# Performance work log

Measured on AMD Instinct MI355X. Metric: run time of the kernel, lower is better.

## Reference

```python
import jax, jax.numpy as jnp
import numpy as np

N_NODES = 100000
N_EDGES = 1600000
D_IN = 128
D_OUT = 128


def setup_inputs() -> dict:
    key = jax.random.key(0)
    k1, k2, k3, k4, k5, k6 = jax.random.split(key, 6)
    x = jax.random.normal(k1, (N_NODES, D_IN), dtype=jnp.float32)
    rows = jax.random.randint(k2, (N_EDGES,), 0, N_NODES, dtype=jnp.int32)
    cols = jax.random.randint(k3, (N_EDGES,), 0, N_NODES, dtype=jnp.int32)
    vals = jax.random.uniform(k4, (N_EDGES,), dtype=jnp.float32)
    # nn.Linear init: U(-1/sqrt(in), 1/sqrt(in))
    bound = 1.0 / np.sqrt(D_IN)
    W = jax.random.uniform(k5, (D_IN, D_OUT), minval=-bound, maxval=bound, dtype=jnp.float32)
    b = jax.random.uniform(k6, (D_OUT,), minval=-bound, maxval=bound, dtype=jnp.float32)
    return {"x": x, "rows": rows, "cols": cols, "vals": vals, "W": W, "b": b}


def reference(x, rows, cols, vals, W, b):
    # support = fc1(x)  -> [N, D_OUT]
    support = x @ W + b
    # output = adj @ support, adj in COO form (rows, cols, vals)
    msg = support[cols] * vals[:, None]          # [E, D_OUT] gather + scale
    out = jax.ops.segment_sum(msg, rows, num_segments=N_NODES)  # scatter-add
    return out
```

## Files before the change

kernel.cpp:

```cpp
#include <hip/hip_runtime.h>

#define D 128
#define NB_MAX 1024
#define CHN 6250
#define CAP 2560
#define SP 136

typedef short short8 __attribute__((ext_vector_type(8)));
typedef float floatx4 __attribute__((ext_vector_type(4)));

__device__ inline unsigned short f2bf(float f) {
  unsigned u = __float_as_uint(f);
  u += 0x7fffu + ((u >> 16) & 1u);
  return (unsigned short)(u >> 16);
}

__global__ __launch_bounds__(1024) void prep_kernel(
    const float* __restrict__ W, unsigned short* __restrict__ wf,
    const float* __restrict__ x, unsigned short* __restrict__ xh,
    const int* __restrict__ rows, int* __restrict__ chunk_hist,
    int n_edges, int nchunks, int nb, int total_elems) {
  __shared__ int h[NB_MAX];
  const int bid = blockIdx.x;
  const int t = threadIdx.x;

  if (bid < nchunks) {
    h[t] = 0;
    __syncthreads();
    int lo = bid * CHN;
    int hi = min(lo + CHN, n_edges);
    for (int i = lo + t; i < hi; i += 1024) atomicAdd(&h[rows[i] >> 7], 1);
    __syncthreads();
    if (t < nb) chunk_hist[bid * nb + t] = h[t];
    return;
  }

  if (bid < nchunks + 2) {
    int tid = (bid - nchunks) * 1024 + t;
    int ks = tid >> 9;
    int rem = tid & 511;
    int nt = rem >> 6;
    int lane = rem & 63;
    int n = nt * 16 + (lane & 15);
    int k0 = ks * 32 + (lane >> 4) * 8;
    unsigned short v[8];
#pragma unroll
    for (int j = 0; j < 8; ++j) v[j] = f2bf(W[(k0 + j) * D + n]);
    uint4 o;
    o.x = (unsigned)v[0] | ((unsigned)v[1] << 16);
    o.y = (unsigned)v[2] | ((unsigned)v[3] << 16);
    o.z = (unsigned)v[4] | ((unsigned)v[5] << 16);
    o.w = (unsigned)v[6] | ((unsigned)v[7] << 16);
    ((uint4*)wf)[tid] = o;
    return;
  }

  int idx = (bid - nchunks - 2) * 1024 + t;
  if (idx * 16 < total_elems) {
    const float4* x4 = (const float4*)x;
    uint4* xh4 = (uint4*)xh;
#pragma unroll
    for (int j = 0; j < 2; ++j) {
      float4 a = x4[idx * 4 + 2 * j];
      float4 c = x4[idx * 4 + 2 * j + 1];
      uint4 o;
      o.x = (unsigned)f2bf(a.x) | ((unsigned)f2bf(a.y) << 16);
      o.y = (unsigned)f2bf(a.z) | ((unsigned)f2bf(a.w) << 16);
      o.z = (unsigned)f2bf(c.x) | ((unsigned)f2bf(c.y) << 16);
      o.w = (unsigned)f2bf(c.z) | ((unsigned)f2bf(c.w) << 16);
      xh4[idx * 2 + j] = o;
    }
  }
}

__global__ __launch_bounds__(1024) void partition_kernel(
    const int* __restrict__ rows, const int* __restrict__ cols,
    const float* __restrict__ vals, const int* __restrict__ chunk_hist,
    int* __restrict__ bucket_off, int2* __restrict__ tmp,
    int n_edges, int nchunks, int nb) {
  __shared__ int pscn[NB_MAX];
  __shared__ int h[NB_MAX];
  __shared__ int base_s[NB_MAX];
  const int c = blockIdx.x;
  const int t = threadIdx.x;

  int tot = 0, pre = 0;
  if (t < nb) {
    for (int cc = 0; cc < nchunks; ++cc) {
      int v = chunk_hist[cc * nb + t];
      tot += v;
      pre += (cc < c) ? v : 0;
    }
  }
  pscn[t] = (t < nb) ? tot : 0;
  __syncthreads();
  for (int d = 1; d < 1024; d <<= 1) {
    int v = (t >= d) ? pscn[t - d] : 0;
    __syncthreads();
    pscn[t] += v;
    __syncthreads();
  }
  int excl = (t == 0) ? 0 : pscn[t - 1];
  if (c == 0) {
    if (t < nb) bucket_off[t] = excl;
    if (t == 0) bucket_off[nb] = pscn[nb - 1];
  }
  base_s[t] = excl + pre;
  h[t] = 0;
  __syncthreads();

  int lo = c * CHN;
  int hi = min(lo + CHN, n_edges);
  for (int i = lo + t; i < hi; i += 1024) {
    int r = rows[i];
    int bkt = r >> 7;
    int l = atomicAdd(&h[bkt], 1);
    tmp[base_s[bkt] + l] =
        make_int2(((r & 127) << 17) | cols[i], __float_as_int(vals[i]));
  }
}

__global__ __launch_bounds__(1024, 8) void gather_gemm_kernel(
    const uint2* __restrict__ xh, const unsigned short* __restrict__ wf,
    const float* __restrict__ bias, const int* __restrict__ bucket_off,
    const int2* __restrict__ tmp, float* __restrict__ out, int n_nodes) {
  __shared__ __align__(16) char U[67584];
  __shared__ int cnt[128];
  __shared__ int scn[128];
  __shared__ int rs[129];
  __shared__ float rowsum[128];
  unsigned short* ys = (unsigned short*)U;
  int2* ebuf = (int2*)U;
  int2* sbuf = (int2*)(U + 34816);
  unsigned short* wfs = (unsigned short*)(U + 34816);
  const int t = threadIdx.x;
  const int b = blockIdx.x;

  const uint4* wf4 = (const uint4*)wf;
  uint4 wfr0 = wf4[t];
  uint4 wfr1 = wf4[t + 1024];

  const int lo = bucket_off[b];
  const int ne = bucket_off[b + 1] - lo;
  const int slot = t >> 5;
  const int lane = t & 31;

  if (ne <= CAP) {
    if (t < 128) cnt[t] = 0;
    __syncthreads();
    for (int i = t; i < ne; i += 1024) {
      int2 p = tmp[lo + i];
      ebuf[i] = p;
      atomicAdd(&cnt[((unsigned)p.x) >> 17], 1);
    }
    __syncthreads();
    if (t < 128) scn[t] = cnt[t];
    __syncthreads();
#pragma unroll
    for (int d = 1; d < 128; d <<= 1) {
      int v = (t < 128 && t >= d) ? scn[t - d] : 0;
      __syncthreads();
      if (t < 128) scn[t] += v;
      __syncthreads();
    }
    if (t < 128) {
      rs[t] = (t == 0) ? 0 : scn[t - 1];
      cnt[t] = 0;
    }
    __syncthreads();
    if (t == 0) rs[128] = scn[127];
    for (int i = t; i < ne; i += 1024) {
      int2 p = ebuf[i];
      int r = ((unsigned)p.x) >> 17;
      int l = atomicAdd(&cnt[r], 1);
      sbuf[rs[r] + l] = p;
    }
    __syncthreads();
#pragma unroll
    for (int rr = 0; rr < 4; ++rr) {
      int row = slot + (rr << 5);
      int s = rs[row], e = rs[row + 1];
      float4 acc = make_float4(0.f, 0.f, 0.f, 0.f);
      float rsum = 0.f;
      int i = s;
      for (; i + 4 <= e; i += 4) {
        int2 p0 = sbuf[i + 0];
        int2 p1 = sbuf[i + 1];
        int2 p2 = sbuf[i + 2];
        int2 p3 = sbuf[i + 3];
        uint2 s0 = xh[((size_t)(p0.x & 0x1FFFF) << 5) + lane];
        uint2 s1 = xh[((size_t)(p1.x & 0x1FFFF) << 5) + lane];
        uint2 s2 = xh[((size_t)(p2.x & 0x1FFFF) << 5) + lane];
        uint2 s3 = xh[((size_t)(p3.x & 0x1FFFF) << 5) + lane];
        float v0 = __int_as_float(p0.y), v1 = __int_as_float(p1.y);
        float v2 = __int_as_float(p2.y), v3 = __int_as_float(p3.y);
        rsum += v0 + v1 + v2 + v3;
        acc.x += v0 * __uint_as_float(s0.x << 16);
        acc.y += v0 * __uint_as_float(s0.x & 0xffff0000u);
        acc.z += v0 * __uint_as_float(s0.y << 16);
        acc.w += v0 * __uint_as_float(s0.y & 0xffff0000u);
        acc.x += v1 * __uint_as_float(s1.x << 16);
        acc.y += v1 * __uint_as_float(s1.x & 0xffff0000u);
        acc.z += v1 * __uint_as_float(s1.y << 16);
        acc.w += v1 * __uint_as_float(s1.y & 0xffff0000u);
        acc.x += v2 * __uint_as_float(s2.x << 16);
        acc.y += v2 * __uint_as_float(s2.x & 0xffff0000u);
        acc.z += v2 * __uint_as_float(s2.y << 16);
        acc.w += v2 * __uint_as_float(s2.y & 0xffff0000u);
        acc.x += v3 * __uint_as_float(s3.x << 16);
        acc.y += v3 * __uint_as_float(s3.x & 0xffff0000u);
        acc.z += v3 * __uint_as_float(s3.y << 16);
        acc.w += v3 * __uint_as_float(s3.y & 0xffff0000u);
      }
      for (; i < e; ++i) {
        int2 p = sbuf[i];
        float v = __int_as_float(p.y);
        uint2 sv = xh[((size_t)(p.x & 0x1FFFF) << 5) + lane];
        rsum += v;
        acc.x += v * __uint_as_float(sv.x << 16);
        acc.y += v * __uint_as_float(sv.x & 0xffff0000u);
        acc.z += v * __uint_as_float(sv.y << 16);
        acc.w += v * __uint_as_float(sv.y & 0xffff0000u);
      }
      unsigned u0 = (unsigned)f2bf(acc.x) | ((unsigned)f2bf(acc.y) << 16);
      unsigned u1 = (unsigned)f2bf(acc.z) | ((unsigned)f2bf(acc.w) << 16);
      *((uint2*)(ys + row * SP + lane * 4)) = make_uint2(u0, u1);
      if (lane == 0) rowsum[row] = rsum;
    }
  } else {
#pragma unroll
    for (int rr = 0; rr < 4; ++rr) {
      int row = slot + (rr << 5);
      float4 acc = make_float4(0.f, 0.f, 0.f, 0.f);
      float rsum = 0.f;
      for (int i = 0; i < ne; ++i) {
        int2 p = tmp[lo + i];
        if ((int)(((unsigned)p.x) >> 17) != row) continue;
        float v = __int_as_float(p.y);
        uint2 sv = xh[((size_t)(p.x & 0x1FFFF) << 5) + lane];
        rsum += v;
        acc.x += v * __uint_as_float(sv.x << 16);
        acc.y += v * __uint_as_float(sv.x & 0xffff0000u);
        acc.z += v * __uint_as_float(sv.y << 16);
        acc.w += v * __uint_as_float(sv.y & 0xffff0000u);
      }
      unsigned u0 = (unsigned)f2bf(acc.x) | ((unsigned)f2bf(acc.y) << 16);
      unsigned u1 = (unsigned)f2bf(acc.z) | ((unsigned)f2bf(acc.w) << 16);
      *((uint2*)(ys + row * SP + lane * 4)) = make_uint2(u0, u1);
      if (lane == 0) rowsum[row] = rsum;
    }
  }
  __syncthreads();

  uint4* wfs4 = (uint4*)wfs;
  wfs4[t] = wfr0;
  wfs4[t + 1024] = wfr1;
  __syncthreads();

  const int l64 = t & 63;
  const int w = t >> 6;
  const int m = l64 & 15, q = l64 >> 4;
  const int rb = (w & 3) * 32;
  const int cb = (w >> 2) * 32;

  floatx4 acc2[2][2];
#pragma unroll
  for (int rt = 0; rt < 2; ++rt)
#pragma unroll
    for (int ct = 0; ct < 2; ++ct) {
      acc2[rt][ct][0] = 0.f; acc2[rt][ct][1] = 0.f;
      acc2[rt][ct][2] = 0.f; acc2[rt][ct][3] = 0.f;
    }

#pragma unroll
  for (int ks = 0; ks < 4; ++ks) {
    short8 af[2], bfr[2];
#pragma unroll
    for (int rt = 0; rt < 2; ++rt)
      af[rt] = *((const short8*)(ys + (rb + rt * 16 + m) * SP + ks * 32 + q * 8));
#pragma unroll
    for (int ct = 0; ct < 2; ++ct) {
      int nt = (cb >> 4) + ct;
      bfr[ct] = *((const short8*)(wfs + ((ks * 8 + nt) * 64 + l64) * 8));
    }
#pragma unroll
    for (int rt = 0; rt < 2; ++rt)
#pragma unroll
      for (int ct = 0; ct < 2; ++ct)
        acc2[rt][ct] = __builtin_amdgcn_mfma_f32_16x16x32_bf16(
            af[rt], bfr[ct], acc2[rt][ct], 0, 0, 0);
  }

  float b0 = bias[cb + m];
  float b1 = bias[cb + 16 + m];
#pragma unroll
  for (int rt = 0; rt < 2; ++rt)
#pragma unroll
    for (int ct = 0; ct < 2; ++ct) {
      float bc = ct ? b1 : b0;
#pragma unroll
      for (int r = 0; r < 4; ++r) {
        int row = rb + rt * 16 + q * 4 + r;
        int col = cb + ct * 16 + m;
        int node = (b << 7) + row;
        if (node < n_nodes)
          out[(size_t)node * D + col] = acc2[rt][ct][r] + rowsum[row] * bc;
      }
    }
}

extern "C" void kernel_launch(void* const* d_in, const int* in_sizes, int n_in,
                              void* d_out, int out_size, void* d_ws, size_t ws_size,
                              hipStream_t stream) {
  const float* x    = (const float*)d_in[0];
  const int*   rows = (const int*)d_in[1];
  const int*   cols = (const int*)d_in[2];
  const float* vals = (const float*)d_in[3];
  const float* W    = (const float*)d_in[4];
  const float* b    = (const float*)d_in[5];
  float* out = (float*)d_out;

  int n_nodes = in_sizes[0] / D;
  int n_edges = in_sizes[1];
  int nb = (n_nodes + 127) >> 7;
  int nchunks = (n_edges + CHN - 1) / CHN;
  int total_elems = n_nodes * D;

  char* ws = (char*)d_ws;
  unsigned short* xh = (unsigned short*)(ws);
  int2* tmp          = (int2*)(ws + 25600000);
  char* mb           = ws + 38400000;
  int* bucket_off    = (int*)(mb);
  unsigned short* wf = (unsigned short*)(mb + 4096);
  int* chunk_hist    = (int*)out;

  int ncast = (total_elems + 16383) / 16384;
  prep_kernel<<<dim3(nchunks + 2 + ncast), dim3(1024), 0, stream>>>(
      W, wf, x, xh, rows, chunk_hist, n_edges, nchunks, nb, total_elems);

  partition_kernel<<<dim3(nchunks), dim3(1024), 0, stream>>>(
      rows, cols, vals, chunk_hist, bucket_off, tmp, n_edges, nchunks, nb);

  gather_gemm_kernel<<<dim3(nb), dim3(1024), 0, stream>>>(
      (const uint2*)xh, wf, b, bucket_off, tmp, out, n_nodes);
}
```

Baseline: 283.0 us.

## Replace single-pass bucket partition with two-level radix partition and separate x cast

The edge partition by destination bucket now runs in two passes. The first scatters edges into 49 superbuckets of 2048 rows, then a second kernel splits each superbucket into its 16 row buckets, keeping per-chunk order. The goal is to cut the scattered writes across ~782 buckets that made the old single pass poorly coalesced. The bf16 cast of x moves to its own kernel that reuses the tmp1 workspace after partitioning, and the gather inner loop is unrolled from 4 to 8 edges for more memory-level parallelism. The cost is an extra kernel launch plus an extra read and write pass over the edge list.

```diff
diff --git a/kernel.cpp b/kernel.cpp
--- a/kernel.cpp
+++ b/kernel.cpp
@@ -2,7 +2,8 @@
 
 #define D 128
 #define NB_MAX 1024
-#define CHN 6250
+#define NSB_STRIDE 64
+#define CHN 4096
 #define CAP 2560
 #define SP 136
 
@@ -15,28 +16,16 @@
   return (unsigned short)(u >> 16);
 }
 
-__global__ __launch_bounds__(1024) void prep_kernel(
+__global__ __launch_bounds__(256) void prep_kernel(
     const float* __restrict__ W, unsigned short* __restrict__ wf,
-    const float* __restrict__ x, unsigned short* __restrict__ xh,
     const int* __restrict__ rows, int* __restrict__ chunk_hist,
-    int n_edges, int nchunks, int nb, int total_elems) {
+    int* __restrict__ chunk_sb, int n_edges, int nb, int nsb) {
   __shared__ int h[NB_MAX];
   const int bid = blockIdx.x;
   const int t = threadIdx.x;
 
-  if (bid < nchunks) {
-    h[t] = 0;
-    __syncthreads();
-    int lo = bid * CHN;
-    int hi = min(lo + CHN, n_edges);
-    for (int i = lo + t; i < hi; i += 1024) atomicAdd(&h[rows[i] >> 7], 1);
-    __syncthreads();
-    if (t < nb) chunk_hist[bid * nb + t] = h[t];
-    return;
-  }
-
-  if (bid < nchunks + 2) {
-    int tid = (bid - nchunks) * 1024 + t;
+  if (bid < 8) {
+    int tid = bid * 256 + t;
     int ks = tid >> 9;
     int rem = tid & 511;
     int nt = rem >> 6;
@@ -55,68 +44,149 @@
     return;
   }
 
-  int idx = (bid - nchunks - 2) * 1024 + t;
-  if (idx * 16 < total_elems) {
-    const float4* x4 = (const float4*)x;
-    uint4* xh4 = (uint4*)xh;
-#pragma unroll
-    for (int j = 0; j < 2; ++j) {
-      float4 a = x4[idx * 4 + 2 * j];
-      float4 c = x4[idx * 4 + 2 * j + 1];
-      uint4 o;
-      o.x = (unsigned)f2bf(a.x) | ((unsigned)f2bf(a.y) << 16);
-      o.y = (unsigned)f2bf(a.z) | ((unsigned)f2bf(a.w) << 16);
-      o.z = (unsigned)f2bf(c.x) | ((unsigned)f2bf(c.y) << 16);
-      o.w = (unsigned)f2bf(c.z) | ((unsigned)f2bf(c.w) << 16);
-      xh4[idx * 2 + j] = o;
-    }
-  }
-}
-
-__global__ __launch_bounds__(1024) void partition_kernel(
+  int c = bid - 8;
+  for (int i = t; i < NB_MAX; i += 256) h[i] = 0;
+  __syncthreads();
+  int lo = c * CHN;
+  int hi = min(lo + CHN, n_edges);
+  for (int i = lo + t; i < hi; i += 256) atomicAdd(&h[rows[i] >> 7], 1);
+  __syncthreads();
+  for (int b = t; b < nb; b += 256) chunk_hist[c * nb + b] = h[b];
+  if (t < nsb) {
+    int s = 0;
+#pragma unroll
+    for (int k = 0; k < 16; ++k) s += h[t * 16 + k];
+    chunk_sb[c * NSB_STRIDE + t] = s;
+  }
+}
+
+__global__ __launch_bounds__(1024) void p1_kernel(
     const int* __restrict__ rows, const int* __restrict__ cols,
     const float* __restrict__ vals, const int* __restrict__ chunk_hist,
-    int* __restrict__ bucket_off, int2* __restrict__ tmp,
-    int n_edges, int nchunks, int nb) {
-  __shared__ int pscn[NB_MAX];
-  __shared__ int h[NB_MAX];
-  __shared__ int base_s[NB_MAX];
+    const int* __restrict__ chunk_sb, int* __restrict__ bucket_off,
+    int2* __restrict__ tmp1, int n_edges, int nchunks, int nb, int nsb) {
   const int c = blockIdx.x;
   const int t = threadIdx.x;
 
-  int tot = 0, pre = 0;
-  if (t < nb) {
+  if (c == nchunks) {
+    __shared__ int pscn[1024];
+    int tot = 0;
+    if (t < nb)
+      for (int cc = 0; cc < nchunks; ++cc) tot += chunk_hist[cc * nb + t];
+    pscn[t] = (t < nb) ? tot : 0;
+    __syncthreads();
+    for (int d = 1; d < 1024; d <<= 1) {
+      int v = (t >= d) ? pscn[t - d] : 0;
+      __syncthreads();
+      pscn[t] += v;
+      __syncthreads();
+    }
+    if (t < nb) bucket_off[t] = (t == 0) ? 0 : pscn[t - 1];
+    if (t == 0) bucket_off[nb] = pscn[nb - 1];
+    return;
+  }
+
+  __shared__ int sbt[NSB_STRIDE];
+  __shared__ int sbo[NSB_STRIDE];
+  __shared__ int base_s[NSB_STRIDE];
+  __shared__ int h[NSB_STRIDE];
+  if (t < nsb) {
+    int tot = 0, pre = 0;
     for (int cc = 0; cc < nchunks; ++cc) {
-      int v = chunk_hist[cc * nb + t];
+      int v = chunk_sb[cc * NSB_STRIDE + t];
       tot += v;
       pre += (cc < c) ? v : 0;
     }
-  }
-  pscn[t] = (t < nb) ? tot : 0;
-  __syncthreads();
-  for (int d = 1; d < 1024; d <<= 1) {
-    int v = (t >= d) ? pscn[t - d] : 0;
-    __syncthreads();
-    pscn[t] += v;
-    __syncthreads();
-  }
-  int excl = (t == 0) ? 0 : pscn[t - 1];
-  if (c == 0) {
-    if (t < nb) bucket_off[t] = excl;
-    if (t == 0) bucket_off[nb] = pscn[nb - 1];
-  }
-  base_s[t] = excl + pre;
-  h[t] = 0;
+    sbt[t] = tot;
+    base_s[t] = pre;
+    h[t] = 0;
+  }
+  __syncthreads();
+  if (t == 0) {
+    int run = 0;
+    for (int s = 0; s < nsb; ++s) { sbo[s] = run; run += sbt[s]; }
+  }
+  __syncthreads();
+  if (t < nsb) base_s[t] += sbo[t];
   __syncthreads();
 
   int lo = c * CHN;
   int hi = min(lo + CHN, n_edges);
   for (int i = lo + t; i < hi; i += 1024) {
     int r = rows[i];
-    int bkt = r >> 7;
-    int l = atomicAdd(&h[bkt], 1);
-    tmp[base_s[bkt] + l] =
-        make_int2(((r & 127) << 17) | cols[i], __float_as_int(vals[i]));
+    int s = r >> 11;
+    int l = atomicAdd(&h[s], 1);
+    tmp1[base_s[s] + l] =
+        make_int2(((r & 2047) << 17) | cols[i], __float_as_int(vals[i]));
+  }
+}
+
+__global__ __launch_bounds__(1024) void p2_kernel(
+    const int* __restrict__ chunk_hist, const int* __restrict__ chunk_sb,
+    const int* __restrict__ bucket_off, const int2* __restrict__ tmp1,
+    int2* __restrict__ tmp2, int nchunks, int nb, int nsb) {
+  __shared__ int wbase[16];
+  __shared__ int h[16];
+  __shared__ int cnt16[16];
+  __shared__ int ab[2];
+  const int s = blockIdx.x >> 4;
+  const int j = blockIdx.x & 15;
+  const int t = threadIdx.x;
+  const int c0 = (nchunks * j) >> 4;
+  const int c1 = (nchunks * (j + 1)) >> 4;
+
+  if (t < 16) {
+    int b = (s << 4) + t;
+    int pre = 0, cnt = 0;
+    if (b < nb) {
+      for (int cc = 0; cc < c1; ++cc) {
+        int v = chunk_hist[cc * nb + b];
+        pre += (cc < c0) ? v : 0;
+        cnt += (cc >= c0) ? v : 0;
+      }
+      wbase[t] = bucket_off[b] + pre;
+    } else {
+      wbase[t] = 0;
+    }
+    cnt16[t] = cnt;
+    h[t] = 0;
+  }
+  __syncthreads();
+  if (t == 0) {
+    int sbstart = bucket_off[s << 4];
+    int pre_sum = 0, cnt_sum = 0;
+    for (int k = 0; k < 16; ++k) {
+      int b = (s << 4) + k;
+      if (b < nb) pre_sum += wbase[k] - bucket_off[b];
+      cnt_sum += cnt16[k];
+    }
+    ab[0] = sbstart + pre_sum;
+    ab[1] = sbstart + pre_sum + cnt_sum;
+  }
+  __syncthreads();
+  const int a = ab[0], bend = ab[1];
+
+  for (int i = a + t; i < bend; i += 1024) {
+    int2 p = tmp1[i];
+    int bi = (((unsigned)p.x) >> 24) & 15;
+    int l = atomicAdd(&h[bi], 1);
+    tmp2[wbase[bi] + l] = make_int2(p.x & 0x00FFFFFF, p.y);
+  }
+}
+
+__global__ __launch_bounds__(1024) void xcast_kernel(
+    const float* __restrict__ x, unsigned int* __restrict__ xh2, int total4) {
+  const float4* x4 = (const float4*)x;
+  int base = blockIdx.x * 4096;
+#pragma unroll
+  for (int k = 0; k < 4; ++k) {
+    int i = base + k * 1024 + threadIdx.x;
+    if (i < total4) {
+      float4 v = x4[i];
+      unsigned lo = (unsigned)f2bf(v.x) | ((unsigned)f2bf(v.y) << 16);
+      unsigned hi = (unsigned)f2bf(v.z) | ((unsigned)f2bf(v.w) << 16);
+      ((uint2*)xh2)[i] = make_uint2(lo, hi);
+    }
   }
 }
 
@@ -183,18 +253,28 @@
       float4 acc = make_float4(0.f, 0.f, 0.f, 0.f);
       float rsum = 0.f;
       int i = s;
-      for (; i + 4 <= e; i += 4) {
+      for (; i + 8 <= e; i += 8) {
         int2 p0 = sbuf[i + 0];
         int2 p1 = sbuf[i + 1];
         int2 p2 = sbuf[i + 2];
         int2 p3 = sbuf[i + 3];
+        int2 p4 = sbuf[i + 4];
+        int2 p5 = sbuf[i + 5];
+        int2 p6 = sbuf[i + 6];
+        int2 p7 = sbuf[i + 7];
         uint2 s0 = xh[((size_t)(p0.x & 0x1FFFF) << 5) + lane];
         uint2 s1 = xh[((size_t)(p1.x & 0x1FFFF) << 5) + lane];
         uint2 s2 = xh[((size_t)(p2.x & 0x1FFFF) << 5) + lane];
         uint2 s3 = xh[((size_t)(p3.x & 0x1FFFF) << 5) + lane];
+        uint2 s4 = xh[((size_t)(p4.x & 0x1FFFF) << 5) + lane];
+        uint2 s5 = xh[((size_t)(p5.x & 0x1FFFF) << 5) + lane];
+        uint2 s6 = xh[((size_t)(p6.x & 0x1FFFF) << 5) + lane];
+        uint2 s7 = xh[((size_t)(p7.x & 0x1FFFF) << 5) + lane];
         float v0 = __int_as_float(p0.y), v1 = __int_as_float(p1.y);
         float v2 = __int_as_float(p2.y), v3 = __int_as_float(p3.y);
-        rsum += v0 + v1 + v2 + v3;
+        float v4 = __int_as_float(p4.y), v5 = __int_as_float(p5.y);
+        float v6 = __int_as_float(p6.y), v7 = __int_as_float(p7.y);
+        rsum += v0 + v1 + v2 + v3 + v4 + v5 + v6 + v7;
         acc.x += v0 * __uint_as_float(s0.x << 16);
         acc.y += v0 * __uint_as_float(s0.x & 0xffff0000u);
         acc.z += v0 * __uint_as_float(s0.y << 16);
@@ -211,6 +291,22 @@
         acc.y += v3 * __uint_as_float(s3.x & 0xffff0000u);
         acc.z += v3 * __uint_as_float(s3.y << 16);
         acc.w += v3 * __uint_as_float(s3.y & 0xffff0000u);
+        acc.x += v4 * __uint_as_float(s4.x << 16);
+        acc.y += v4 * __uint_as_float(s4.x & 0xffff0000u);
+        acc.z += v4 * __uint_as_float(s4.y << 16);
+        acc.w += v4 * __uint_as_float(s4.y & 0xffff0000u);
+        acc.x += v5 * __uint_as_float(s5.x << 16);
+        acc.y += v5 * __uint_as_float(s5.x & 0xffff0000u);
+        acc.z += v5 * __uint_as_float(s5.y << 16);
+        acc.w += v5 * __uint_as_float(s5.y & 0xffff0000u);
+        acc.x += v6 * __uint_as_float(s6.x << 16);
+        acc.y += v6 * __uint_as_float(s6.x & 0xffff0000u);
+        acc.z += v6 * __uint_as_float(s6.y << 16);
+        acc.w += v6 * __uint_as_float(s6.y & 0xffff0000u);
+        acc.x += v7 * __uint_as_float(s7.x << 16);
+        acc.y += v7 * __uint_as_float(s7.x & 0xffff0000u);
+        acc.z += v7 * __uint_as_float(s7.y << 16);
+        acc.w += v7 * __uint_as_float(s7.y & 0xffff0000u);
       }
       for (; i < e; ++i) {
         int2 p = sbuf[i];
@@ -323,24 +419,34 @@
   int n_nodes = in_sizes[0] / D;
   int n_edges = in_sizes[1];
   int nb = (n_nodes + 127) >> 7;
+  int nsb = (nb + 15) >> 4;
   int nchunks = (n_edges + CHN - 1) / CHN;
   int total_elems = n_nodes * D;
 
   char* ws = (char*)d_ws;
+  int2* tmp1         = (int2*)(ws);
   unsigned short* xh = (unsigned short*)(ws);
-  int2* tmp          = (int2*)(ws + 25600000);
+  int2* tmp2         = (int2*)(ws + 25600000);
   char* mb           = ws + 38400000;
   int* bucket_off    = (int*)(mb);
   unsigned short* wf = (unsigned short*)(mb + 4096);
   int* chunk_hist    = (int*)out;
-
-  int ncast = (total_elems + 16383) / 16384;
-  prep_kernel<<<dim3(nchunks + 2 + ncast), dim3(1024), 0, stream>>>(
-      W, wf, x, xh, rows, chunk_hist, n_edges, nchunks, nb, total_elems);
-
-  partition_kernel<<<dim3(nchunks), dim3(1024), 0, stream>>>(
-      rows, cols, vals, chunk_hist, bucket_off, tmp, n_edges, nchunks, nb);
+  int* chunk_sb      = (int*)((char*)out + 2000000);
+
+  prep_kernel<<<dim3(8 + nchunks), dim3(256), 0, stream>>>(
+      W, wf, rows, chunk_hist, chunk_sb, n_edges, nb, nsb);
+
+  p1_kernel<<<dim3(nchunks + 1), dim3(1024), 0, stream>>>(
+      rows, cols, vals, chunk_hist, chunk_sb, bucket_off, tmp1,
+      n_edges, nchunks, nb, nsb);
+
+  p2_kernel<<<dim3(nsb * 16), dim3(1024), 0, stream>>>(
+      chunk_hist, chunk_sb, bucket_off, tmp1, tmp2, nchunks, nb, nsb);
+
+  int total4 = total_elems >> 2;
+  xcast_kernel<<<dim3((total4 + 4095) / 4096), dim3(1024), 0, stream>>>(
+      x, (unsigned int*)xh, total4);
 
   gather_gemm_kernel<<<dim3(nb), dim3(1024), 0, stream>>>(
-      (const uint2*)xh, wf, b, bucket_off, tmp, out, n_nodes);
-}
+      (const uint2*)xh, wf, b, bucket_off, tmp2, out, n_nodes);
+}
```

Result: slower. 466.5 us (+64.8%).

## Partition edges into coarse 2048-row superbuckets and filter per block in gather kernel

Applied to the files above, without the earlier changes.

Replaces the fine 128-row bucket histogram and partition (782 buckets × 256 chunks) with coarse 2048-row superbuckets (49 of them), making the histogram and prefix-scan work much smaller. Each gather block now scans its whole superbucket and keeps only the edges for its 128-row sub-bucket. Blocks are mapped so that the blocks sharing a superbucket sit on the same XCD to help L2 reuse. The trade-off is that each superbucket's edge list is read 16 times, and the filter adds shared atomics. The bf16 cast of x is also reshaped into per-float4 work items.

```diff
diff --git a/kernel.cpp b/kernel.cpp
--- a/kernel.cpp
+++ b/kernel.cpp
@@ -1,8 +1,9 @@
 #include <hip/hip_runtime.h>
 
 #define D 128
-#define NB_MAX 1024
-#define CHN 6250
+#define SBMAX 64
+#define CSTRIDE 400
+#define CHN 4096
 #define CAP 2560
 #define SP 136
 
@@ -17,26 +18,15 @@
 
 __global__ __launch_bounds__(1024) void prep_kernel(
     const float* __restrict__ W, unsigned short* __restrict__ wf,
-    const float* __restrict__ x, unsigned short* __restrict__ xh,
-    const int* __restrict__ rows, int* __restrict__ chunk_hist,
-    int n_edges, int nchunks, int nb, int total_elems) {
-  __shared__ int h[NB_MAX];
+    const float* __restrict__ x, unsigned int* __restrict__ xh2,
+    const int* __restrict__ rows, int* __restrict__ chunk_sb,
+    int n_edges, int nchunks, int nsb, int total4) {
+  __shared__ int h[SBMAX];
   const int bid = blockIdx.x;
   const int t = threadIdx.x;
 
-  if (bid < nchunks) {
-    h[t] = 0;
-    __syncthreads();
-    int lo = bid * CHN;
-    int hi = min(lo + CHN, n_edges);
-    for (int i = lo + t; i < hi; i += 1024) atomicAdd(&h[rows[i] >> 7], 1);
-    __syncthreads();
-    if (t < nb) chunk_hist[bid * nb + t] = h[t];
-    return;
-  }
-
-  if (bid < nchunks + 2) {
-    int tid = (bid - nchunks) * 1024 + t;
+  if (bid < 2) {
+    int tid = bid * 1024 + t;
     int ks = tid >> 9;
     int rem = tid & 511;
     int nt = rem >> 6;
@@ -55,105 +45,144 @@
     return;
   }
 
-  int idx = (bid - nchunks - 2) * 1024 + t;
-  if (idx * 16 < total_elems) {
-    const float4* x4 = (const float4*)x;
-    uint4* xh4 = (uint4*)xh;
-#pragma unroll
-    for (int j = 0; j < 2; ++j) {
-      float4 a = x4[idx * 4 + 2 * j];
-      float4 c = x4[idx * 4 + 2 * j + 1];
-      uint4 o;
-      o.x = (unsigned)f2bf(a.x) | ((unsigned)f2bf(a.y) << 16);
-      o.y = (unsigned)f2bf(a.z) | ((unsigned)f2bf(a.w) << 16);
-      o.z = (unsigned)f2bf(c.x) | ((unsigned)f2bf(c.y) << 16);
-      o.w = (unsigned)f2bf(c.z) | ((unsigned)f2bf(c.w) << 16);
-      xh4[idx * 2 + j] = o;
-    }
-  }
-}
-
-__global__ __launch_bounds__(1024) void partition_kernel(
+  if (bid < 2 + nchunks) {
+    if (t < SBMAX) h[t] = 0;
+    __syncthreads();
+    int c = bid - 2;
+    int lo = c * CHN;
+    int hi = min(lo + CHN, n_edges);
+    for (int i = lo + t; i < hi; i += 1024) atomicAdd(&h[rows[i] >> 11], 1);
+    __syncthreads();
+    if (t < nsb) chunk_sb[t * CSTRIDE + c] = h[t];
+    return;
+  }
+
+  const float4* x4 = (const float4*)x;
+  int base = (bid - 2 - nchunks) * 4096;
+#pragma unroll
+  for (int k = 0; k < 4; ++k) {
+    int i = base + k * 1024 + t;
+    if (i < total4) {
+      float4 v = x4[i];
+      unsigned lo = (unsigned)f2bf(v.x) | ((unsigned)f2bf(v.y) << 16);
+      unsigned hi = (unsigned)f2bf(v.z) | ((unsigned)f2bf(v.w) << 16);
+      ((uint2*)xh2)[i] = make_uint2(lo, hi);
+    }
+  }
+}
+
+__global__ __launch_bounds__(1024) void p1_kernel(
     const int* __restrict__ rows, const int* __restrict__ cols,
-    const float* __restrict__ vals, const int* __restrict__ chunk_hist,
-    int* __restrict__ bucket_off, int2* __restrict__ tmp,
-    int n_edges, int nchunks, int nb) {
-  __shared__ int pscn[NB_MAX];
-  __shared__ int h[NB_MAX];
-  __shared__ int base_s[NB_MAX];
+    const float* __restrict__ vals, const int* __restrict__ chunk_sb,
+    int* __restrict__ sb_off, int2* __restrict__ tmp1,
+    int n_edges, int nchunks, int nsb) {
+  __shared__ int ptot[1024];
+  __shared__ int ppre[1024];
+  __shared__ int sbt[SBMAX];
+  __shared__ int sbo[SBMAX + 1];
+  __shared__ int base_s[SBMAX];
+  __shared__ int h[SBMAX];
   const int c = blockIdx.x;
   const int t = threadIdx.x;
 
-  int tot = 0, pre = 0;
-  if (t < nb) {
-    for (int cc = 0; cc < nchunks; ++cc) {
-      int v = chunk_hist[cc * nb + t];
-      tot += v;
-      pre += (cc < c) ? v : 0;
-    }
-  }
-  pscn[t] = (t < nb) ? tot : 0;
-  __syncthreads();
-  for (int d = 1; d < 1024; d <<= 1) {
-    int v = (t >= d) ? pscn[t - d] : 0;
-    __syncthreads();
-    pscn[t] += v;
-    __syncthreads();
-  }
-  int excl = (t == 0) ? 0 : pscn[t - 1];
-  if (c == 0) {
-    if (t < nb) bucket_off[t] = excl;
-    if (t == 0) bucket_off[nb] = pscn[nb - 1];
-  }
-  base_s[t] = excl + pre;
-  h[t] = 0;
+  {
+    int s = t >> 4, g = t & 15;
+    int tp = 0, pp = 0;
+    if (s < nsb) {
+      int strip = (nchunks + 15) >> 4;
+      int a = g * strip;
+      int b2 = min(a + strip, nchunks);
+      const int* rowp = chunk_sb + s * CSTRIDE;
+      for (int cc = a; cc < b2; ++cc) {
+        int v = rowp[cc];
+        tp += v;
+        pp += (cc < c) ? v : 0;
+      }
+    }
+    ptot[t] = tp;
+    ppre[t] = pp;
+  }
+  __syncthreads();
+  if (t < nsb) {
+    int tp = 0, pp = 0;
+#pragma unroll
+    for (int g = 0; g < 16; ++g) { tp += ptot[(t << 4) + g]; pp += ppre[(t << 4) + g]; }
+    sbt[t] = tp;
+    base_s[t] = pp;
+    h[t] = 0;
+  }
+  __syncthreads();
+  if (t == 0) {
+    int run = 0;
+    for (int s = 0; s < nsb; ++s) { sbo[s] = run; run += sbt[s]; }
+    sbo[nsb] = run;
+  }
+  __syncthreads();
+  if (t < nsb) base_s[t] += sbo[t];
+  if (c == 0 && t <= nsb) sb_off[t] = sbo[t];
   __syncthreads();
 
   int lo = c * CHN;
   int hi = min(lo + CHN, n_edges);
   for (int i = lo + t; i < hi; i += 1024) {
     int r = rows[i];
-    int bkt = r >> 7;
-    int l = atomicAdd(&h[bkt], 1);
-    tmp[base_s[bkt] + l] =
-        make_int2(((r & 127) << 17) | cols[i], __float_as_int(vals[i]));
+    int s = r >> 11;
+    int l = atomicAdd(&h[s], 1);
+    tmp1[base_s[s] + l] =
+        make_int2(((r & 2047) << 17) | cols[i], __float_as_int(vals[i]));
   }
 }
 
 __global__ __launch_bounds__(1024, 8) void gather_gemm_kernel(
     const uint2* __restrict__ xh, const unsigned short* __restrict__ wf,
-    const float* __restrict__ bias, const int* __restrict__ bucket_off,
-    const int2* __restrict__ tmp, float* __restrict__ out, int n_nodes) {
+    const float* __restrict__ bias, const int* __restrict__ sb_off,
+    const int2* __restrict__ tmp1, float* __restrict__ out,
+    int n_nodes, int nsb) {
   __shared__ __align__(16) char U[67584];
   __shared__ int cnt[128];
   __shared__ int scn[128];
   __shared__ int rs[129];
   __shared__ float rowsum[128];
+  __shared__ int fc;
   unsigned short* ys = (unsigned short*)U;
   int2* ebuf = (int2*)U;
   int2* sbuf = (int2*)(U + 34816);
   unsigned short* wfs = (unsigned short*)(U + 34816);
   const int t = threadIdx.x;
-  const int b = blockIdx.x;
+
+  const int xcd = blockIdx.x & 7;
+  const int mg = blockIdx.x >> 3;
+  const int jj = mg & 15;
+  const int sbi = (mg >> 4) * 8 + xcd;
+  if (sbi >= nsb) return;
+  const int node0 = ((sbi << 4) + jj) << 7;
+  if (node0 >= n_nodes) return;
 
   const uint4* wf4 = (const uint4*)wf;
   uint4 wfr0 = wf4[t];
   uint4 wfr1 = wf4[t + 1024];
 
-  const int lo = bucket_off[b];
-  const int ne = bucket_off[b + 1] - lo;
+  const int lo = sb_off[sbi];
+  const int rne = sb_off[sbi + 1] - lo;
   const int slot = t >> 5;
   const int lane = t & 31;
 
+  if (t < 128) cnt[t] = 0;
+  if (t == 0) fc = 0;
+  __syncthreads();
+  for (int i = t; i < rne; i += 1024) {
+    int2 p = tmp1[lo + i];
+    int lr = ((unsigned)p.x) >> 17;
+    if ((lr >> 7) == jj) {
+      int pos = atomicAdd(&fc, 1);
+      if (pos < CAP) ebuf[pos] = p;
+      atomicAdd(&cnt[lr & 127], 1);
+    }
+  }
+  __syncthreads();
+  const int ne = fc;
+
   if (ne <= CAP) {
-    if (t < 128) cnt[t] = 0;
-    __syncthreads();
-    for (int i = t; i < ne; i += 1024) {
-      int2 p = tmp[lo + i];
-      ebuf[i] = p;
-      atomicAdd(&cnt[((unsigned)p.x) >> 17], 1);
-    }
-    __syncthreads();
     if (t < 128) scn[t] = cnt[t];
     __syncthreads();
 #pragma unroll
@@ -171,7 +200,7 @@
     if (t == 0) rs[128] = scn[127];
     for (int i = t; i < ne; i += 1024) {
       int2 p = ebuf[i];
-      int r = ((unsigned)p.x) >> 17;
+      int r = (((unsigned)p.x) >> 17) & 127;
       int l = atomicAdd(&cnt[r], 1);
       sbuf[rs[r] + l] = p;
     }
@@ -231,11 +260,12 @@
 #pragma unroll
     for (int rr = 0; rr < 4; ++rr) {
       int row = slot + (rr << 5);
+      int tgt = (jj << 7) | row;
       float4 acc = make_float4(0.f, 0.f, 0.f, 0.f);
       float rsum = 0.f;
-      for (int i = 0; i < ne; ++i) {
-        int2 p = tmp[lo + i];
-        if ((int)(((unsigned)p.x) >> 17) != row) continue;
+      for (int i = 0; i < rne; ++i) {
+        int2 p = tmp1[lo + i];
+        if ((int)(((unsigned)p.x) >> 17) != tgt) continue;
         float v = __int_as_float(p.y);
         uint2 sv = xh[((size_t)(p.x & 0x1FFFF) << 5) + lane];
         rsum += v;
@@ -302,7 +332,7 @@
       for (int r = 0; r < 4; ++r) {
         int row = rb + rt * 16 + q * 4 + r;
         int col = cb + ct * 16 + m;
-        int node = (b << 7) + row;
+        int node = node0 + row;
         if (node < n_nodes)
           out[(size_t)node * D + col] = acc2[rt][ct][r] + rowsum[row] * bc;
       }
@@ -323,24 +353,28 @@
   int n_nodes = in_sizes[0] / D;
   int n_edges = in_sizes[1];
   int nb = (n_nodes + 127) >> 7;
+  int nsb = (nb + 15) >> 4;
   int nchunks = (n_edges + CHN - 1) / CHN;
   int total_elems = n_nodes * D;
+  int total4 = total_elems >> 2;
 
   char* ws = (char*)d_ws;
   unsigned short* xh = (unsigned short*)(ws);
-  int2* tmp          = (int2*)(ws + 25600000);
+  int2* tmp1         = (int2*)(ws + 25600000);
   char* mb           = ws + 38400000;
-  int* bucket_off    = (int*)(mb);
-  unsigned short* wf = (unsigned short*)(mb + 4096);
-  int* chunk_hist    = (int*)out;
-
-  int ncast = (total_elems + 16383) / 16384;
-  prep_kernel<<<dim3(nchunks + 2 + ncast), dim3(1024), 0, stream>>>(
-      W, wf, x, xh, rows, chunk_hist, n_edges, nchunks, nb, total_elems);
-
-  partition_kernel<<<dim3(nchunks), dim3(1024), 0, stream>>>(
-      rows, cols, vals, chunk_hist, bucket_off, tmp, n_edges, nchunks, nb);
-
-  gather_gemm_kernel<<<dim3(nb), dim3(1024), 0, stream>>>(
-      (const uint2*)xh, wf, b, bucket_off, tmp, out, n_nodes);
-}
+  int* sb_off        = (int*)(mb);
+  unsigned short* wf = (unsigned short*)(mb + 512);
+  int* chunk_sb      = (int*)out;
+
+  int cblocks = (total4 + 4095) / 4096;
+  prep_kernel<<<dim3(2 + nchunks + cblocks), dim3(1024), 0, stream>>>(
+      W, wf, x, (unsigned int*)xh, rows, chunk_sb,
+      n_edges, nchunks, nsb, total4);
+
+  p1_kernel<<<dim3(nchunks), dim3(1024), 0, stream>>>(
+      rows, cols, vals, chunk_sb, sb_off, tmp1, n_edges, nchunks, nsb);
+
+  int ggrid = ((nsb + 7) >> 3) * 8 * 16;
+  gather_gemm_kernel<<<dim3(ggrid), dim3(1024), 0, stream>>>(
+      (const uint2*)xh, wf, b, sb_off, tmp1, out, n_nodes, nsb);
+}
```

Measured after the change: 236.5 us. 1.2x faster.
